# Kernel tuning notes

Measured on AMD Instinct MI355X. Metric: run time of the kernel, lower is better.

Reference implementation:

```python
import jax, jax.numpy as jnp
import numpy as np

H, W = 1024, 1024
DOMAIN_W, DOMAIN_H = 1.0, 1.0
DX2 = (DOMAIN_W / (W - 1)) ** 2
DY2 = (DOMAIN_H / (H - 1)) ** 2
DU0, DV0 = 0.16, 0.08
DT = 0.1 * min(DX2, DY2) / (4.0 * max(DU0, DV0))


def setup_inputs() -> dict:
    # Initial condition per reset_state(): U=1, V=0, with a central disk set to 0.5
    U = np.ones((1, 1, H, W), dtype=np.float32)
    V = np.zeros((1, 1, H, W), dtype=np.float32)
    cx, cy = W // 2, H // 2
    dx = DOMAIN_W / (W - 1)
    dy = DOMAIN_H / (H - 1)
    radius_grid = 0.1 * min(DOMAIN_W, DOMAIN_H) / min(dx, dy)
    y, x = np.meshgrid(np.arange(H), np.arange(W), indexing='ij')
    mask = (x - cx) ** 2 + (y - cy) ** 2 <= radius_grid ** 2
    U[0, 0, mask] = 0.5
    V[0, 0, mask] = 0.5
    return {
        'U_init': jnp.asarray(U),
        'V_init': jnp.asarray(V),
        'log_Du': jnp.asarray(np.log(DU0), dtype=jnp.float32),
        'log_Dv': jnp.asarray(np.log(DV0), dtype=jnp.float32),
        'f': jnp.float32(0.02),
        'k': jnp.float32(0.051),
        'steps': 64,
    }


def _laplacian(Z):
    # periodic 5-point stencil via roll (axes: (1,1,H,W))
    d2x = (jnp.roll(Z, 1, axis=3) - 2.0 * Z + jnp.roll(Z, -1, axis=3)) / DX2
    d2y = (jnp.roll(Z, 1, axis=2) - 2.0 * Z + jnp.roll(Z, -1, axis=2)) / DY2
    return d2x + d2y


def reference(U_init, V_init, log_Du, log_Dv, f, k, steps):
    Du = jnp.clip(jnp.exp(log_Du), 0.001, 1.0)
    Dv = jnp.clip(jnp.exp(log_Dv), 0.001, 1.0)

    def step(carry, _):
        U, V = carry
        U = jnp.clip(U, 0.0, 2.0)
        V = jnp.clip(V, 0.0, 2.0)
        Lu = jnp.clip(_laplacian(U), -10.0, 10.0)
        Lv = jnp.clip(_laplacian(V), -10.0, 10.0)
        uvv = U * V * V
        du = jnp.clip(Du * Lu - uvv + f * (1.0 - U), -1.0, 1.0)
        dv = jnp.clip(Dv * Lv + uvv - (f + k) * V, -1.0, 1.0)
        U_new = jnp.clip(U + du * DT, 0.0, 2.0)
        V_new = jnp.clip(V + dv * DT, 0.0, 2.0)
        return (U_new, V_new), None

    (U_fin, V_fin), _ = jax.lax.scan(step, (U_init, V_init), None, length=steps)
    return jnp.stack([U_fin, V_fin])  # (2,1,1,H,W)
```

## Files before the change

kernel.cpp:

```cpp
#include <hip/hip_runtime.h>
#include <math.h>

namespace {

constexpr int H = 1024;
constexpr int W = 1024;
constexpr int HW = H * W;
constexpr int STEPS = 64;
constexpr int TILE = 64;
constexpr int HALO = 8;
constexpr int P = TILE + 2 * HALO;
constexpr int TSTEP = 8;
constexpr int NLAUNCH = STEPS / TSTEP;
constexpr int NTX = W / TILE;
constexpr int NTHREADS = 512;
constexpr int PITCH = P + 2;

__device__ __forceinline__ float clampf(float v, float lo, float hi) {
    return fminf(fmaxf(v, lo), hi);
}

__global__ __launch_bounds__(NTHREADS) void gs_tile(
    const float* __restrict__ Uin, const float* __restrict__ Vin,
    float* __restrict__ Uout, float* __restrict__ Vout,
    const float* __restrict__ pLogDu, const float* __restrict__ pLogDv,
    const float* __restrict__ pf, const float* __restrict__ pk,
    float invDX2, float invDY2, float dt)
{
    __shared__ __align__(16) float2 sUV[2][P * PITCH];

    const int tid = threadIdx.x;
    const int bx = blockIdx.x & (NTX - 1);
    const int by = blockIdx.x >> 4;
    const int gx0 = bx * TILE - HALO;
    const int gy0 = by * TILE - HALO;

    const float Du = clampf(expf(pLogDu[0]), 0.001f, 1.0f);
    const float Dv = clampf(expf(pLogDv[0]), 0.001f, 1.0f);
    const float f = pf[0], k = pk[0];
    const float fk = f + k;

    for (int t = tid; t < P * (P / 4); t += NTHREADS) {
        const int r  = t / (P / 4);
        const int c4 = (t - r * (P / 4)) * 4;
        const int gy = (gy0 + r) & (H - 1);
        const int gx = (gx0 + c4) & (W - 1);
        const float4 u4 = *reinterpret_cast<const float4*>(Uin + gy * W + gx);
        const float4 v4 = *reinterpret_cast<const float4*>(Vin + gy * W + gx);
        float4* dst = reinterpret_cast<float4*>(&sUV[0][r * PITCH + c4]);
        dst[0] = make_float4(clampf(u4.x, 0.f, 2.f), clampf(v4.x, 0.f, 2.f),
                             clampf(u4.y, 0.f, 2.f), clampf(v4.y, 0.f, 2.f));
        dst[1] = make_float4(clampf(u4.z, 0.f, 2.f), clampf(v4.z, 0.f, 2.f),
                             clampf(u4.w, 0.f, 2.f), clampf(v4.w, 0.f, 2.f));
    }
    __syncthreads();

    int b = 0;
#pragma unroll
    for (int s = 1; s <= TSTEP; ++s) {
        const float2* __restrict__ cb = sUV[b];
        float2* __restrict__ nb = sUV[b ^ 1];

        const int rlo   = s;
        const int nrows = P - 2 * s;
        const int c4lo  = s & ~3;
        const int c4hi  = (P - 1 - s) & ~3;
        const int nc    = (c4hi - c4lo) / 4 + 1;
        const int tasks = nrows * nc;

        for (int t = tid; t < tasks; t += NTHREADS) {
            const int rr  = t / nc;
            const int row = rlo + rr;
            const int c4  = c4lo + (t - rr * nc) * 4;

            const float2* rC = cb + row * PITCH;
            const float2* rN = rC - PITCH;
            const float2* rS = rC + PITCH;
            const int lc = (c4 > 0) ? c4 - 1 : 0;
            const int rc = (c4 + 4 < P) ? c4 + 4 : P - 1;

            const float4 c01 = *reinterpret_cast<const float4*>(rC + c4);
            const float4 c23 = *reinterpret_cast<const float4*>(rC + c4 + 2);
            const float4 n01 = *reinterpret_cast<const float4*>(rN + c4);
            const float4 n23 = *reinterpret_cast<const float4*>(rN + c4 + 2);
            const float4 s01 = *reinterpret_cast<const float4*>(rS + c4);
            const float4 s23 = *reinterpret_cast<const float4*>(rS + c4 + 2);
            const float2 eL = rC[lc];
            const float2 eR = rC[rc];

            const float u[6]   = { eL.x, c01.x, c01.z, c23.x, c23.z, eR.x };
            const float v[6]   = { eL.y, c01.y, c01.w, c23.y, c23.w, eR.y };
            const float unn[4] = { n01.x, n01.z, n23.x, n23.z };
            const float vnn[4] = { n01.y, n01.w, n23.y, n23.w };
            const float uss[4] = { s01.x, s01.z, s23.x, s23.z };
            const float vss[4] = { s01.y, s01.w, s23.y, s23.w };

            float ou[4], ov[4];
#pragma unroll
            for (int e = 0; e < 4; ++e) {
                const float uc = u[e + 1];
                const float vc = v[e + 1];
                float lu = (u[e] + u[e + 2] - 2.0f * uc) * invDX2
                         + (unn[e] + uss[e] - 2.0f * uc) * invDY2;
                float lv = (v[e] + v[e + 2] - 2.0f * vc) * invDX2
                         + (vnn[e] + vss[e] - 2.0f * vc) * invDY2;
                lu = clampf(lu, -10.0f, 10.0f);
                lv = clampf(lv, -10.0f, 10.0f);
                const float uvv = uc * vc * vc;
                const float du = clampf(fmaf(Du, lu, fmaf(f, 1.0f - uc, -uvv)), -1.0f, 1.0f);
                const float dv = clampf(fmaf(Dv, lv, uvv - fk * vc), -1.0f, 1.0f);
                ou[e] = clampf(fmaf(du, dt, uc), 0.0f, 2.0f);
                ov[e] = clampf(fmaf(dv, dt, vc), 0.0f, 2.0f);
            }
            float4* dst = reinterpret_cast<float4*>(nb + row * PITCH + c4);
            dst[0] = make_float4(ou[0], ov[0], ou[1], ov[1]);
            dst[1] = make_float4(ou[2], ov[2], ou[3], ov[3]);
        }
        b ^= 1;
        __syncthreads();
    }

    const float2* __restrict__ fb = sUV[b];
    for (int i = tid; i < TILE * (TILE / 4); i += NTHREADS) {
        const int r  = i / (TILE / 4);
        const int c4 = (i - r * (TILE / 4)) * 4;
        const float4* src = reinterpret_cast<const float4*>(
            fb + (r + HALO) * PITCH + (c4 + HALO));
        const float4 a = src[0];
        const float4 bq = src[1];
        const int go = (by * TILE + r) * W + bx * TILE + c4;
        *reinterpret_cast<float4*>(Uout + go) = make_float4(a.x, a.z, bq.x, bq.z);
        *reinterpret_cast<float4*>(Vout + go) = make_float4(a.y, a.w, bq.y, bq.w);
    }
}

}

extern "C" void kernel_launch(void* const* d_in, const int* in_sizes, int n_in,
                              void* d_out, int out_size, void* d_ws, size_t ws_size,
                              hipStream_t stream) {
    const float* U0     = (const float*)d_in[0];
    const float* V0     = (const float*)d_in[1];
    const float* pLogDu = (const float*)d_in[2];
    const float* pLogDv = (const float*)d_in[3];
    const float* pf     = (const float*)d_in[4];
    const float* pk     = (const float*)d_in[5];

    float* wsU  = (float*)d_ws;
    float* wsV  = wsU + HW;
    float* outU = (float*)d_out;
    float* outV = outU + HW;

    const double dx  = 1.0 / (W - 1);
    const double dy  = 1.0 / (H - 1);
    const double dx2 = dx * dx;
    const double dy2 = dy * dy;
    const float invdx2 = (float)(1.0 / dx2);
    const float invdy2 = (float)(1.0 / dy2);
    const float dtf    = (float)(0.1 * ((dx2 < dy2) ? dx2 : dy2) / (4.0 * 0.16));

    const int grid = (H / TILE) * (W / TILE);

    const float* cu = U0;
    const float* cv = V0;
    for (int l = 0; l < NLAUNCH; ++l) {
        float* nu;
        float* nv;
        if (l & 1) { nu = outU; nv = outV; }
        else       { nu = wsU;  nv = wsV;  }
        gs_tile<<<grid, NTHREADS, 0, stream>>>(cu, cv, nu, nv,
                                               pLogDu, pLogDv, pf, pk,
                                               invdx2, invdy2, dtf);
        cu = nu; cv = nv;
    }
}
```

Measured before the change: 148.6 us.

## Fuse all launches into one cooperative kernel with grid sync and register row-walking

Replaces the eight separate temporally blocked launches with a single cooperative kernel that loops over phases and uses grid.sync between them, removing per-launch overhead. The inner stencil now walks rows per thread, carrying north and center rows in registers so only the south row is reloaded from shared memory. Cooperative launch requires all 256 blocks to be co-resident, and grid-wide barriers add their own synchronization cost. Row-walking can also reduce parallelism per step.

```diff
diff --git a/kernel.cpp b/kernel.cpp
--- a/kernel.cpp
+++ b/kernel.cpp
@@ -1,17 +1,19 @@
 #include <hip/hip_runtime.h>
+#include <hip/hip_cooperative_groups.h>
 #include <math.h>
+
+namespace cg = cooperative_groups;
 
 namespace {
 
 constexpr int H = 1024;
 constexpr int W = 1024;
 constexpr int HW = H * W;
-constexpr int STEPS = 64;
 constexpr int TILE = 64;
 constexpr int HALO = 8;
 constexpr int P = TILE + 2 * HALO;
 constexpr int TSTEP = 8;
-constexpr int NLAUNCH = STEPS / TSTEP;
+constexpr int NPHASE = 8;
 constexpr int NTX = W / TILE;
 constexpr int NTHREADS = 512;
 constexpr int PITCH = P + 2;
@@ -19,10 +21,14 @@
 __device__ __forceinline__ float clampf(float v, float lo, float hi) {
     return fminf(fmaxf(v, lo), hi);
 }
+__device__ __forceinline__ float4 ld4(const float2* p) {
+    return *reinterpret_cast<const float4*>(p);
+}
 
-__global__ __launch_bounds__(NTHREADS) void gs_tile(
-    const float* __restrict__ Uin, const float* __restrict__ Vin,
-    float* __restrict__ Uout, float* __restrict__ Vout,
+__global__ __launch_bounds__(NTHREADS, 1) void gs_fused(
+    const float* __restrict__ U0, const float* __restrict__ V0,
+    float* __restrict__ wsU, float* __restrict__ wsV,
+    float* __restrict__ outU, float* __restrict__ outV,
     const float* __restrict__ pLogDu, const float* __restrict__ pLogDv,
     const float* __restrict__ pf, const float* __restrict__ pk,
     float invDX2, float invDY2, float dt)
@@ -40,97 +46,120 @@
     const float f = pf[0], k = pk[0];
     const float fk = f + k;
 
-    for (int t = tid; t < P * (P / 4); t += NTHREADS) {
-        const int r  = t / (P / 4);
-        const int c4 = (t - r * (P / 4)) * 4;
-        const int gy = (gy0 + r) & (H - 1);
-        const int gx = (gx0 + c4) & (W - 1);
-        const float4 u4 = *reinterpret_cast<const float4*>(Uin + gy * W + gx);
-        const float4 v4 = *reinterpret_cast<const float4*>(Vin + gy * W + gx);
-        float4* dst = reinterpret_cast<float4*>(&sUV[0][r * PITCH + c4]);
-        dst[0] = make_float4(clampf(u4.x, 0.f, 2.f), clampf(v4.x, 0.f, 2.f),
-                             clampf(u4.y, 0.f, 2.f), clampf(v4.y, 0.f, 2.f));
-        dst[1] = make_float4(clampf(u4.z, 0.f, 2.f), clampf(v4.z, 0.f, 2.f),
-                             clampf(u4.w, 0.f, 2.f), clampf(v4.w, 0.f, 2.f));
-    }
-    __syncthreads();
+    cg::grid_group grid = cg::this_grid();
 
-    int b = 0;
+    for (int p = 0; p < NPHASE; ++p) {
+        const float* __restrict__ srcU = (p == 0) ? U0 : ((p & 1) ? wsU : outU);
+        const float* __restrict__ srcV = (p == 0) ? V0 : ((p & 1) ? wsV : outV);
+        float* __restrict__ dstU = (p & 1) ? outU : wsU;
+        float* __restrict__ dstV = (p & 1) ? outV : wsV;
+
+        for (int t = tid; t < P * (P / 4); t += NTHREADS) {
+            const int r  = t / (P / 4);
+            const int c4 = (t - r * (P / 4)) * 4;
+            const int gy = (gy0 + r) & (H - 1);
+            const int gx = (gx0 + c4) & (W - 1);
+            const float4 u4 = *reinterpret_cast<const float4*>(srcU + gy * W + gx);
+            const float4 v4 = *reinterpret_cast<const float4*>(srcV + gy * W + gx);
+            float4* dst = reinterpret_cast<float4*>(&sUV[0][r * PITCH + c4]);
+            dst[0] = make_float4(clampf(u4.x, 0.f, 2.f), clampf(v4.x, 0.f, 2.f),
+                                 clampf(u4.y, 0.f, 2.f), clampf(v4.y, 0.f, 2.f));
+            dst[1] = make_float4(clampf(u4.z, 0.f, 2.f), clampf(v4.z, 0.f, 2.f),
+                                 clampf(u4.w, 0.f, 2.f), clampf(v4.w, 0.f, 2.f));
+        }
+        __syncthreads();
+
+        int b = 0;
 #pragma unroll
-    for (int s = 1; s <= TSTEP; ++s) {
-        const float2* __restrict__ cb = sUV[b];
-        float2* __restrict__ nb = sUV[b ^ 1];
+        for (int s = 1; s <= TSTEP; ++s) {
+            const float2* __restrict__ cb = sUV[b];
+            float2* __restrict__ nb = sUV[b ^ 1];
 
-        const int rlo   = s;
-        const int nrows = P - 2 * s;
-        const int c4lo  = s & ~3;
-        const int c4hi  = (P - 1 - s) & ~3;
-        const int nc    = (c4hi - c4lo) / 4 + 1;
-        const int tasks = nrows * nc;
+            const int rlo   = s;
+            const int nrows = P - 2 * s;
+            const int c4lo  = s & ~3;
+            const int c4hi  = (P - 1 - s) & ~3;
+            const int nc    = (c4hi - c4lo) / 4 + 1;
+            const int nwalk = NTHREADS / nc;
+            const int itmax = (nrows + nwalk - 1) / nwalk;
 
-        for (int t = tid; t < tasks; t += NTHREADS) {
-            const int rr  = t / nc;
-            const int row = rlo + rr;
-            const int c4  = c4lo + (t - rr * nc) * 4;
-
-            const float2* rC = cb + row * PITCH;
-            const float2* rN = rC - PITCH;
-            const float2* rS = rC + PITCH;
+            const int col = tid % nc;
+            const int wk  = tid / nc;
+            const bool active = (wk < nwalk);
+            const int r0 = rlo + (nrows * wk) / nwalk;
+            const int r1 = rlo + (nrows * (wk + 1)) / nwalk;
+            const int c4 = c4lo + col * 4;
             const int lc = (c4 > 0) ? c4 - 1 : 0;
             const int rc = (c4 + 4 < P) ? c4 + 4 : P - 1;
 
-            const float4 c01 = *reinterpret_cast<const float4*>(rC + c4);
-            const float4 c23 = *reinterpret_cast<const float4*>(rC + c4 + 2);
-            const float4 n01 = *reinterpret_cast<const float4*>(rN + c4);
-            const float4 n23 = *reinterpret_cast<const float4*>(rN + c4 + 2);
-            const float4 s01 = *reinterpret_cast<const float4*>(rS + c4);
-            const float4 s23 = *reinterpret_cast<const float4*>(rS + c4 + 2);
-            const float2 eL = rC[lc];
-            const float2 eR = rC[rc];
+            float4 n01, n23, c01, c23;
+            if (active) {
+                const float2* rN = cb + (r0 - 1) * PITCH;
+                const float2* rC = cb + r0 * PITCH;
+                n01 = ld4(rN + c4); n23 = ld4(rN + c4 + 2);
+                c01 = ld4(rC + c4); c23 = ld4(rC + c4 + 2);
+            }
+#pragma unroll
+            for (int it = 0; it < itmax; ++it) {
+                const int r = r0 + it;
+                if (active && r < r1) {
+                    const float2* rS = cb + (r + 1) * PITCH;
+                    const float2* rC = cb + r * PITCH;
+                    const float4 s01 = ld4(rS + c4);
+                    const float4 s23 = ld4(rS + c4 + 2);
+                    const float2 eL = rC[lc];
+                    const float2 eR = rC[rc];
 
-            const float u[6]   = { eL.x, c01.x, c01.z, c23.x, c23.z, eR.x };
-            const float v[6]   = { eL.y, c01.y, c01.w, c23.y, c23.w, eR.y };
-            const float unn[4] = { n01.x, n01.z, n23.x, n23.z };
-            const float vnn[4] = { n01.y, n01.w, n23.y, n23.w };
-            const float uss[4] = { s01.x, s01.z, s23.x, s23.z };
-            const float vss[4] = { s01.y, s01.w, s23.y, s23.w };
+                    const float u[6]   = { eL.x, c01.x, c01.z, c23.x, c23.z, eR.x };
+                    const float v[6]   = { eL.y, c01.y, c01.w, c23.y, c23.w, eR.y };
+                    const float unn[4] = { n01.x, n01.z, n23.x, n23.z };
+                    const float vnn[4] = { n01.y, n01.w, n23.y, n23.w };
+                    const float uss[4] = { s01.x, s01.z, s23.x, s23.z };
+                    const float vss[4] = { s01.y, s01.w, s23.y, s23.w };
 
-            float ou[4], ov[4];
+                    float ou[4], ov[4];
 #pragma unroll
-            for (int e = 0; e < 4; ++e) {
-                const float uc = u[e + 1];
-                const float vc = v[e + 1];
-                float lu = (u[e] + u[e + 2] - 2.0f * uc) * invDX2
-                         + (unn[e] + uss[e] - 2.0f * uc) * invDY2;
-                float lv = (v[e] + v[e + 2] - 2.0f * vc) * invDX2
-                         + (vnn[e] + vss[e] - 2.0f * vc) * invDY2;
-                lu = clampf(lu, -10.0f, 10.0f);
-                lv = clampf(lv, -10.0f, 10.0f);
-                const float uvv = uc * vc * vc;
-                const float du = clampf(fmaf(Du, lu, fmaf(f, 1.0f - uc, -uvv)), -1.0f, 1.0f);
-                const float dv = clampf(fmaf(Dv, lv, uvv - fk * vc), -1.0f, 1.0f);
-                ou[e] = clampf(fmaf(du, dt, uc), 0.0f, 2.0f);
-                ov[e] = clampf(fmaf(dv, dt, vc), 0.0f, 2.0f);
+                    for (int e = 0; e < 4; ++e) {
+                        const float uc = u[e + 1];
+                        const float vc = v[e + 1];
+                        float lu = (u[e] + u[e + 2] - 2.0f * uc) * invDX2
+                                 + (unn[e] + uss[e] - 2.0f * uc) * invDY2;
+                        float lv = (v[e] + v[e + 2] - 2.0f * vc) * invDX2
+                                 + (vnn[e] + vss[e] - 2.0f * vc) * invDY2;
+                        lu = clampf(lu, -10.0f, 10.0f);
+                        lv = clampf(lv, -10.0f, 10.0f);
+                        const float uvv = uc * vc * vc;
+                        const float du = clampf(fmaf(Du, lu, fmaf(f, 1.0f - uc, -uvv)), -1.0f, 1.0f);
+                        const float dv = clampf(fmaf(Dv, lv, uvv - fk * vc), -1.0f, 1.0f);
+                        ou[e] = clampf(fmaf(du, dt, uc), 0.0f, 2.0f);
+                        ov[e] = clampf(fmaf(dv, dt, vc), 0.0f, 2.0f);
+                    }
+                    float4* dst = reinterpret_cast<float4*>(nb + r * PITCH + c4);
+                    dst[0] = make_float4(ou[0], ov[0], ou[1], ov[1]);
+                    dst[1] = make_float4(ou[2], ov[2], ou[3], ov[3]);
+
+                    n01 = c01; n23 = c23;
+                    c01 = s01; c23 = s23;
+                }
             }
-            float4* dst = reinterpret_cast<float4*>(nb + row * PITCH + c4);
-            dst[0] = make_float4(ou[0], ov[0], ou[1], ov[1]);
-            dst[1] = make_float4(ou[2], ov[2], ou[3], ov[3]);
+            __syncthreads();
+            b ^= 1;
         }
-        b ^= 1;
-        __syncthreads();
-    }
 
-    const float2* __restrict__ fb = sUV[b];
-    for (int i = tid; i < TILE * (TILE / 4); i += NTHREADS) {
-        const int r  = i / (TILE / 4);
-        const int c4 = (i - r * (TILE / 4)) * 4;
-        const float4* src = reinterpret_cast<const float4*>(
-            fb + (r + HALO) * PITCH + (c4 + HALO));
-        const float4 a = src[0];
-        const float4 bq = src[1];
-        const int go = (by * TILE + r) * W + bx * TILE + c4;
-        *reinterpret_cast<float4*>(Uout + go) = make_float4(a.x, a.z, bq.x, bq.z);
-        *reinterpret_cast<float4*>(Vout + go) = make_float4(a.y, a.w, bq.y, bq.w);
+        const float2* __restrict__ fb = sUV[b];
+        for (int i = tid; i < TILE * (TILE / 4); i += NTHREADS) {
+            const int r  = i / (TILE / 4);
+            const int c4 = (i - r * (TILE / 4)) * 4;
+            const float4* src = reinterpret_cast<const float4*>(
+                fb + (r + HALO) * PITCH + (c4 + HALO));
+            const float4 a = src[0];
+            const float4 q = src[1];
+            const int go = (by * TILE + r) * W + bx * TILE + c4;
+            *reinterpret_cast<float4*>(dstU + go) = make_float4(a.x, a.z, q.x, q.z);
+            *reinterpret_cast<float4*>(dstV + go) = make_float4(a.y, a.w, q.y, q.w);
+        }
+
+        if (p != NPHASE - 1) grid.sync();
     }
 }
 
@@ -155,22 +184,16 @@
     const double dy  = 1.0 / (H - 1);
     const double dx2 = dx * dx;
     const double dy2 = dy * dy;
-    const float invdx2 = (float)(1.0 / dx2);
-    const float invdy2 = (float)(1.0 / dy2);
-    const float dtf    = (float)(0.1 * ((dx2 < dy2) ? dx2 : dy2) / (4.0 * 0.16));
+    float invdx2 = (float)(1.0 / dx2);
+    float invdy2 = (float)(1.0 / dy2);
+    float dtf    = (float)(0.1 * ((dx2 < dy2) ? dx2 : dy2) / (4.0 * 0.16));
 
-    const int grid = (H / TILE) * (W / TILE);
-
-    const float* cu = U0;
-    const float* cv = V0;
-    for (int l = 0; l < NLAUNCH; ++l) {
-        float* nu;
-        float* nv;
-        if (l & 1) { nu = outU; nv = outV; }
-        else       { nu = wsU;  nv = wsV;  }
-        gs_tile<<<grid, NTHREADS, 0, stream>>>(cu, cv, nu, nv,
-                                               pLogDu, pLogDv, pf, pk,
-                                               invdx2, invdy2, dtf);
-        cu = nu; cv = nv;
-    }
+    void* args[] = {
+        (void*)&U0, (void*)&V0, (void*)&wsU, (void*)&wsV, (void*)&outU, (void*)&outV,
+        (void*)&pLogDu, (void*)&pLogDv, (void*)&pf, (void*)&pk,
+        (void*)&invdx2, (void*)&invdy2, (void*)&dtf
+    };
+    hipLaunchCooperativeKernel((const void*)gs_fused,
+                               dim3((H / TILE) * (W / TILE)), dim3(NTHREADS),
+                               args, 0, stream);
 }
```

Result: slower. 381.1 us (+156.4%).

## Deepen temporal blocking to 16 steps and compute two rows per thread

Applied to the files above, without the earlier changes.

The halo and per-launch step count are doubled, so the kernel runs 4 launches instead of 8 and global round-trips are halved. Each thread now updates a vertical pair of rows, so the middle rows' shared-memory loads are reused for both outputs, cutting LDS reads per output. Per-step column bounds are now compile-time constants and the block size rises to 1024 threads. In exchange, the redundant halo computation grows and the larger tile needs about 150KB of LDS per block, which limits occupancy to one block per CU.

```diff
diff --git a/kernel.cpp b/kernel.cpp
--- a/kernel.cpp
+++ b/kernel.cpp
@@ -8,16 +8,19 @@
 constexpr int HW = H * W;
 constexpr int STEPS = 64;
 constexpr int TILE = 64;
-constexpr int HALO = 8;
+constexpr int HALO = 16;
 constexpr int P = TILE + 2 * HALO;
-constexpr int TSTEP = 8;
+constexpr int TSTEP = 16;
 constexpr int NLAUNCH = STEPS / TSTEP;
 constexpr int NTX = W / TILE;
-constexpr int NTHREADS = 512;
+constexpr int NTHREADS = 1024;
 constexpr int PITCH = P + 2;
 
 __device__ __forceinline__ float clampf(float v, float lo, float hi) {
     return fminf(fmaxf(v, lo), hi);
+}
+__device__ __forceinline__ float4 ld4(const float2* p) {
+    return *reinterpret_cast<const float4*>(p);
 }
 
 __global__ __launch_bounds__(NTHREADS) void gs_tile(
@@ -56,69 +59,87 @@
     __syncthreads();
 
     int b = 0;
-#pragma unroll
-    for (int s = 1; s <= TSTEP; ++s) {
-        const float2* __restrict__ cb = sUV[b];
-        float2* __restrict__ nb = sUV[b ^ 1];
 
-        const int rlo   = s;
-        const int nrows = P - 2 * s;
-        const int c4lo  = s & ~3;
-        const int c4hi  = (P - 1 - s) & ~3;
-        const int nc    = (c4hi - c4lo) / 4 + 1;
-        const int tasks = nrows * nc;
+#define GS_STEP(S, NC, C4LO)                                                     \
+    {                                                                            \
+        const float2* __restrict__ cb = sUV[b];                                  \
+        float2* __restrict__ nb = sUV[b ^ 1];                                    \
+        const int rlo   = (S);                                                   \
+        const int npair = (P - 2 * (S)) >> 1;                                    \
+        const int tasks = npair * (NC);                                          \
+        for (int t = tid; t < tasks; t += NTHREADS) {                            \
+            const int pr  = t / (NC);                \
+            const int row = rlo + 2 * pr;                                        \
+            const int c4  = (C4LO) + (t - pr * (NC)) * 4;                        \
+            const float2* rA = cb + row * PITCH;                                 \
+            const float2* rN = rA - PITCH;                                       \
+            const float2* rB = rA + PITCH;                                       \
+            const float2* rS = rB + PITCH;                                       \
+            const int lc = (c4 > 0) ? c4 - 1 : 0;                                \
+            const int rc = (c4 + 4 < P) ? c4 + 4 : P - 1;                        \
+            const float4 n01 = ld4(rN + c4), n23 = ld4(rN + c4 + 2);             \
+            const float4 a01 = ld4(rA + c4), a23 = ld4(rA + c4 + 2);             \
+            const float4 b01 = ld4(rB + c4), b23 = ld4(rB + c4 + 2);             \
+            const float4 s01 = ld4(rS + c4), s23 = ld4(rS + c4 + 2);             \
+            const float2 eLa = rA[lc], eRa = rA[rc];                             \
+            const float2 eLb = rB[lc], eRb = rB[rc];                             \
+            const float ua[6]  = { eLa.x, a01.x, a01.z, a23.x, a23.z, eRa.x };   \
+            const float va[6]  = { eLa.y, a01.y, a01.w, a23.y, a23.w, eRa.y };   \
+            const float ub[6]  = { eLb.x, b01.x, b01.z, b23.x, b23.z, eRb.x };   \
+            const float vb[6]  = { eLb.y, b01.y, b01.w, b23.y, b23.w, eRb.y };   \
+            const float unn[4] = { n01.x, n01.z, n23.x, n23.z };                 \
+            const float vnn[4] = { n01.y, n01.w, n23.y, n23.w };                 \
+            const float uss[4] = { s01.x, s01.z, s23.x, s23.z };                 \
+            const float vss[4] = { s01.y, s01.w, s23.y, s23.w };                 \
+            float oua[4], ova[4], oub[4], ovb[4];                                \
+            _Pragma("unroll")                                                    \
+            for (int e = 0; e < 4; ++e) {                                        \
+                {                                                                \
+                    const float uc = ua[e + 1], vc = va[e + 1];                  \
+                    float lu = (ua[e] + ua[e + 2] - 2.0f * uc) * invDX2          \
+                             + (unn[e] + ub[e + 1] - 2.0f * uc) * invDY2;        \
+                    float lv = (va[e] + va[e + 2] - 2.0f * vc) * invDX2          \
+                             + (vnn[e] + vb[e + 1] - 2.0f * vc) * invDY2;        \
+                    lu = clampf(lu, -10.0f, 10.0f);                              \
+                    lv = clampf(lv, -10.0f, 10.0f);                              \
+                    const float uvv = uc * vc * vc;                              \
+                    const float du = clampf(fmaf(Du, lu, fmaf(f, 1.0f - uc, -uvv)), -1.0f, 1.0f); \
+                    const float dv = clampf(fmaf(Dv, lv, uvv - fk * vc), -1.0f, 1.0f);            \
+                    oua[e] = clampf(fmaf(du, dt, uc), 0.0f, 2.0f);               \
+                    ova[e] = clampf(fmaf(dv, dt, vc), 0.0f, 2.0f);               \
+                }                                                                \
+                {                                                                \
+                    const float uc = ub[e + 1], vc = vb[e + 1];                  \
+                    float lu = (ub[e] + ub[e + 2] - 2.0f * uc) * invDX2          \
+                             + (ua[e + 1] + uss[e] - 2.0f * uc) * invDY2;        \
+                    float lv = (vb[e] + vb[e + 2] - 2.0f * vc) * invDX2          \
+                             + (va[e + 1] + vss[e] - 2.0f * vc) * invDY2;        \
+                    lu = clampf(lu, -10.0f, 10.0f);                              \
+                    lv = clampf(lv, -10.0f, 10.0f);                              \
+                    const float uvv = uc * vc * vc;                              \
+                    const float du = clampf(fmaf(Du, lu, fmaf(f, 1.0f - uc, -uvv)), -1.0f, 1.0f); \
+                    const float dv = clampf(fmaf(Dv, lv, uvv - fk * vc), -1.0f, 1.0f);            \
+                    oub[e] = clampf(fmaf(du, dt, uc), 0.0f, 2.0f);               \
+                    ovb[e] = clampf(fmaf(dv, dt, vc), 0.0f, 2.0f);               \
+                }                                                                \
+            }                                                                    \
+            float4* dstA = reinterpret_cast<float4*>(nb + row * PITCH + c4);     \
+            dstA[0] = make_float4(oua[0], ova[0], oua[1], ova[1]);               \
+            dstA[1] = make_float4(oua[2], ova[2], oua[3], ova[3]);               \
+            float4* dstB = reinterpret_cast<float4*>(nb + (row + 1) * PITCH + c4); \
+            dstB[0] = make_float4(oub[0], ovb[0], oub[1], ovb[1]);               \
+            dstB[1] = make_float4(oub[2], ovb[2], oub[3], ovb[3]);               \
+        }                                                                        \
+        b ^= 1;                                                                  \
+        __syncthreads();                                                         \
+    }
 
-        for (int t = tid; t < tasks; t += NTHREADS) {
-            const int rr  = t / nc;
-            const int row = rlo + rr;
-            const int c4  = c4lo + (t - rr * nc) * 4;
-
-            const float2* rC = cb + row * PITCH;
-            const float2* rN = rC - PITCH;
-            const float2* rS = rC + PITCH;
-            const int lc = (c4 > 0) ? c4 - 1 : 0;
-            const int rc = (c4 + 4 < P) ? c4 + 4 : P - 1;
-
-            const float4 c01 = *reinterpret_cast<const float4*>(rC + c4);
-            const float4 c23 = *reinterpret_cast<const float4*>(rC + c4 + 2);
-            const float4 n01 = *reinterpret_cast<const float4*>(rN + c4);
-            const float4 n23 = *reinterpret_cast<const float4*>(rN + c4 + 2);
-            const float4 s01 = *reinterpret_cast<const float4*>(rS + c4);
-            const float4 s23 = *reinterpret_cast<const float4*>(rS + c4 + 2);
-            const float2 eL = rC[lc];
-            const float2 eR = rC[rc];
-
-            const float u[6]   = { eL.x, c01.x, c01.z, c23.x, c23.z, eR.x };
-            const float v[6]   = { eL.y, c01.y, c01.w, c23.y, c23.w, eR.y };
-            const float unn[4] = { n01.x, n01.z, n23.x, n23.z };
-            const float vnn[4] = { n01.y, n01.w, n23.y, n23.w };
-            const float uss[4] = { s01.x, s01.z, s23.x, s23.z };
-            const float vss[4] = { s01.y, s01.w, s23.y, s23.w };
-
-            float ou[4], ov[4];
-#pragma unroll
-            for (int e = 0; e < 4; ++e) {
-                const float uc = u[e + 1];
-                const float vc = v[e + 1];
-                float lu = (u[e] + u[e + 2] - 2.0f * uc) * invDX2
-                         + (unn[e] + uss[e] - 2.0f * uc) * invDY2;
-                float lv = (v[e] + v[e + 2] - 2.0f * vc) * invDX2
-                         + (vnn[e] + vss[e] - 2.0f * vc) * invDY2;
-                lu = clampf(lu, -10.0f, 10.0f);
-                lv = clampf(lv, -10.0f, 10.0f);
-                const float uvv = uc * vc * vc;
-                const float du = clampf(fmaf(Du, lu, fmaf(f, 1.0f - uc, -uvv)), -1.0f, 1.0f);
-                const float dv = clampf(fmaf(Dv, lv, uvv - fk * vc), -1.0f, 1.0f);
-                ou[e] = clampf(fmaf(du, dt, uc), 0.0f, 2.0f);
-                ov[e] = clampf(fmaf(dv, dt, vc), 0.0f, 2.0f);
-            }
-            float4* dst = reinterpret_cast<float4*>(nb + row * PITCH + c4);
-            dst[0] = make_float4(ou[0], ov[0], ou[1], ov[1]);
-            dst[1] = make_float4(ou[2], ov[2], ou[3], ov[3]);
-        }
-        b ^= 1;
-        __syncthreads();
-    }
+    for (int s = 1; s <= 3; ++s)   GS_STEP(s,  24,  0);
+    for (int s = 4; s <= 7; ++s)   GS_STEP(s,  22,  4);
+    for (int s = 8; s <= 11; ++s)  GS_STEP(s,  20,  8);
+    for (int s = 12; s <= 15; ++s) GS_STEP(s,  18, 12);
+    GS_STEP(16, 16, 16);
+#undef GS_STEP
 
     const float2* __restrict__ fb = sUV[b];
     for (int i = tid; i < TILE * (TILE / 4); i += NTHREADS) {
@@ -127,10 +148,10 @@
         const float4* src = reinterpret_cast<const float4*>(
             fb + (r + HALO) * PITCH + (c4 + HALO));
         const float4 a = src[0];
-        const float4 bq = src[1];
+        const float4 q = src[1];
         const int go = (by * TILE + r) * W + bx * TILE + c4;
-        *reinterpret_cast<float4*>(Uout + go) = make_float4(a.x, a.z, bq.x, bq.z);
-        *reinterpret_cast<float4*>(Vout + go) = make_float4(a.y, a.w, bq.y, bq.w);
+        *reinterpret_cast<float4*>(Uout + go) = make_float4(a.x, a.z, q.x, q.z);
+        *reinterpret_cast<float4*>(Vout + go) = make_float4(a.y, a.w, q.y, q.w);
     }
 }
 
```

Result: faster. 133.8 us (-10.0%).
